# Kernel optimization log

Measured on AMD Instinct MI355X. Metric: run time of the kernel, lower is better.

Reference implementation:

```python
import jax, jax.numpy as jnp
import numpy as np

N, D, G = 16384, 2048, 4096  # points, vocab_size (feature dim), num_groups


def setup_inputs() -> dict:
    key = jax.random.key(0)
    kx, ke = jax.random.split(key)
    x = jax.random.normal(kx, (N, D), dtype=jnp.float32)
    # trunc_normal_ init for the codebook; plain normal is fine for a numeric reference
    emb = jax.random.truncated_normal(ke, -2.0, 2.0, (G, D), dtype=jnp.float32)
    return {"x": x, "emb": emb}


def reference(x, emb):
    x2 = jnp.sum(x * x, axis=-1, keepdims=True)          # [N, 1]
    e2 = jnp.sum(emb * emb, axis=-1)                     # [G]
    sq = x2 + e2[None, :] - 2.0 * (x @ emb.T)            # [N, G]
    dist = jnp.sqrt(jnp.maximum(sq, 0.0))
    return -dist
```

## Files before the change

### kernel.cpp

```cpp
#include <hip/hip_runtime.h>
#include <hip/hip_bf16.h>

#define NPTS 16384
#define DIM  2048
#define NGRP 4096
#define BK   32
#define NT   (DIM / BK)

typedef __bf16 bf16x8 __attribute__((ext_vector_type(8)));
typedef unsigned short u16x8 __attribute__((ext_vector_type(8)));
typedef float f32x4 __attribute__((ext_vector_type(4)));
typedef long long i64f8;

__device__ __forceinline__ unsigned short f2bf(float f) {
  union { float f; unsigned u; } v; v.f = f;
  unsigned u = v.u;
  return (unsigned short)((u + 0x7FFFu + ((u >> 16) & 1u)) >> 16);
}
__device__ __forceinline__ float bflo(unsigned u) { return __uint_as_float(u << 16); }
__device__ __forceinline__ float bfhi(unsigned u) { return __uint_as_float(u & 0xffff0000u); }

__device__ __forceinline__ unsigned cvtpk4(float a, float b, float c, float d) {
  int w = __builtin_amdgcn_cvt_pk_fp8_f32(a, b, 0, false);
  w = __builtin_amdgcn_cvt_pk_fp8_f32(c, d, w, true);
  return (unsigned)w;
}

__device__ __forceinline__ void gload16(const void* g, void* lds) {
  __builtin_amdgcn_global_load_lds(
      (const __attribute__((address_space(1))) unsigned*)g,
      (__attribute__((address_space(3))) unsigned*)lds, 16, 0, 0);
}

__device__ __forceinline__ bool sniff_bf16(const void* X) {
  const int lane = threadIdx.x & 63;
  unsigned hb = (((const unsigned short*)X)[lane] >> 8) & 0x7Fu;
  unsigned long long m = __ballot(hb >= 0x3Bu && hb <= 0x41u);
  return __popcll(m) >= 48;
}

__global__ __launch_bounds__(256) void prep_all_kernel(
    const void* __restrict__ Xin, const void* __restrict__ Ein,
    unsigned char* __restrict__ Xf8, unsigned char* __restrict__ Ef8,
    float* __restrict__ x2, float* __restrict__ e2) {
  const int lane  = threadIdx.x & 63;
  const int wavei = threadIdx.x >> 6;
  const bool isbf = sniff_bf16(Xin);

  const int grow = blockIdx.x * 4 + wavei;
  const void* in; unsigned char* q; float* nrm; int row;
  if (grow < NPTS) { in = Xin; q = Xf8; nrm = x2; row = grow; }
  else             { in = Ein; q = Ef8; nrm = e2; row = grow - NPTS; }

  unsigned char* qq = q + (size_t)row * DIM;
  float s = 0.f;
#pragma unroll
  for (int it = 0; it < 4; ++it) {
    float v0, v1, v2, v3, v4, v5, v6, v7;
    if (isbf) {
      const unsigned short* p = (const unsigned short*)in + (size_t)row * DIM;
      uint4 r = *(const uint4*)(p + it * 512 + lane * 8);
      v0 = bflo(r.x); v1 = bfhi(r.x); v2 = bflo(r.y); v3 = bfhi(r.y);
      v4 = bflo(r.z); v5 = bfhi(r.z); v6 = bflo(r.w); v7 = bfhi(r.w);
    } else {
      const float* p = (const float*)in + (size_t)row * DIM;
      float4 a = *(const float4*)(p + it * 512 + lane * 8);
      float4 b = *(const float4*)(p + it * 512 + lane * 8 + 4);
      v0 = a.x; v1 = a.y; v2 = a.z; v3 = a.w;
      v4 = b.x; v5 = b.y; v6 = b.z; v7 = b.w;
    }
    s += v0 * v0 + v1 * v1 + v2 * v2 + v3 * v3;
    s += v4 * v4 + v5 * v5 + v6 * v6 + v7 * v7;
    uint2 w;
    w.x = cvtpk4(v0, v1, v2, v3);
    w.y = cvtpk4(v4, v5, v6, v7);
    *(uint2*)(qq + it * 512 + lane * 8) = w;
  }
#pragma unroll
  for (int off = 32; off > 0; off >>= 1) s += __shfl_down(s, off, 64);
  if (lane == 0) nrm[row] = s;
}

__global__ __launch_bounds__(512, 2) void gemm_f8_kernel(
    const void* __restrict__ Xin,
    const unsigned char* __restrict__ X8, const unsigned char* __restrict__ E8,
    const float* __restrict__ x2, const float* __restrict__ e2,
    void* __restrict__ outv) {
  __shared__ __align__(16) unsigned char sbuf[4][16384];

  const int tid  = threadIdx.x;
  const int lane = tid & 63;
  const int wave = tid >> 6;
  const int wm   = wave >> 2;
  const int wn   = wave & 3;
  const int quad = lane >> 4;
  const int l16  = lane & 15;

  const bool isbf = sniff_bf16(Xin);

  const int rowBase = blockIdx.y * 256;
  const int colBase = blockIdx.x * 256;

  const size_t gA = (size_t)(rowBase + (tid >> 1)) * DIM + (tid & 1) * 16;
  const size_t gB = (size_t)(colBase + (tid >> 1)) * DIM + (tid & 1) * 16;

  const int aoff = (wm * 128 + l16) * 32 + quad * 8;
  const int boff = 8192 + (wn * 64 + l16) * 32 + quad * 8;

  f32x4 zero = {0.f, 0.f, 0.f, 0.f};
  f32x4 acc[8][4];
#pragma unroll
  for (int mt = 0; mt < 8; ++mt)
#pragma unroll
    for (int nt = 0; nt < 4; ++nt) acc[mt][nt] = zero;

  i64f8 a0[8], b0[4], a1[8], b1[4];

#define STAGE(t_) do {                                                          \
    gload16(X8 + gA + (size_t)(t_) * BK, &sbuf[(t_) & 3][wave * 1024]);         \
    gload16(E8 + gB + (size_t)(t_) * BK, &sbuf[(t_) & 3][8192 + wave * 1024]);  \
  } while (0)

#define DSR(t_, A_, B_) do { const unsigned char* sb_ = sbuf[(t_) & 3];         \
    _Pragma("unroll") for (int mt = 0; mt < 8; ++mt)                            \
      A_[mt] = *(const i64f8*)(const void*)(sb_ + aoff + mt * 512);             \
    _Pragma("unroll") for (int nt = 0; nt < 4; ++nt)                            \
      B_[nt] = *(const i64f8*)(const void*)(sb_ + boff + nt * 512);             \
  } while (0)

#define MFMA32(A_, B_) do {                                                     \
    __builtin_amdgcn_s_setprio(1);                                              \
    _Pragma("unroll") for (int mt = 0; mt < 8; ++mt)                            \
      _Pragma("unroll") for (int nt = 0; nt < 4; ++nt)                          \
        acc[mt][nt] = __builtin_amdgcn_mfma_f32_16x16x32_fp8_fp8(               \
            A_[mt], B_[nt], acc[mt][nt], 0, 0, 0);                              \
    __builtin_amdgcn_s_setprio(0);                                              \
    asm volatile("" ::: "memory");                                              \
  } while (0)

#define BODY(t_, DOSTAGE_, VMS_, A_, B_, DONEXT_, AN_, BN_, LKS_) do {          \
    asm volatile("s_waitcnt vmcnt(" VMS_ ")" ::: "memory");                     \
    __builtin_amdgcn_s_barrier();                                               \
    __builtin_amdgcn_sched_barrier(0);                                          \
    if (DOSTAGE_) STAGE((t_) + 3);                                              \
    if (DONEXT_) DSR((t_) + 1, AN_, BN_);                                       \
    __builtin_amdgcn_sched_barrier(0);                                          \
    asm volatile("s_waitcnt lgkmcnt(" LKS_ ")" ::: "memory");                   \
    __builtin_amdgcn_sched_barrier(0);                                          \
    MFMA32(A_, B_);                                                             \
  } while (0)

  STAGE(0); STAGE(1); STAGE(2);
  asm volatile("s_waitcnt vmcnt(4)" ::: "memory");
  __builtin_amdgcn_s_barrier();
  __builtin_amdgcn_sched_barrier(0);
  DSR(0, a0, b0);
  __builtin_amdgcn_sched_barrier(0);

#pragma unroll 1
  for (int p = 0; p < 29; ++p) {
    const int t = 2 * p;
    BODY(t,     true, "2", a0, b0, true, a1, b1, "12");
    BODY(t + 1, true, "2", a1, b1, true, a0, b0, "12");
  }
  BODY(58, true,  "2", a0, b0, true, a1, b1, "12");
  BODY(59, true,  "2", a1, b1, true, a0, b0, "12");
  BODY(60, true,  "2", a0, b0, true, a1, b1, "12");
  BODY(61, false, "2", a1, b1, true, a0, b0, "12");
  BODY(62, false, "0", a0, b0, true, a1, b1, "12");
  BODY(63, false, "0", a1, b1, false, a0, b0, "0");
#undef BODY
#undef MFMA32
#undef DSR
#undef STAGE

  float ec[4];
#pragma unroll
  for (int nt = 0; nt < 4; ++nt) ec[nt] = e2[colBase + wn * 64 + nt * 16 + l16];

  if (isbf) {
    unsigned short* out = (unsigned short*)outv;
#pragma unroll
    for (int mt = 0; mt < 8; ++mt)
#pragma unroll
      for (int r2 = 0; r2 < 4; ++r2) {
        const int row = rowBase + wm * 128 + mt * 16 + quad * 4 + r2;
        const float xr = x2[row];
#pragma unroll
        for (int nt = 0; nt < 4; ++nt) {
          const int col = colBase + wn * 64 + nt * 16 + l16;
          float sq = xr + ec[nt] - 2.0f * acc[mt][nt][r2];
          sq = sq > 0.f ? sq : 0.f;
          out[(size_t)row * NGRP + col] = f2bf(-__builtin_sqrtf(sq));
        }
      }
  } else {
    float* out = (float*)outv;
#pragma unroll
    for (int mt = 0; mt < 8; ++mt)
#pragma unroll
      for (int r2 = 0; r2 < 4; ++r2) {
        const int row = rowBase + wm * 128 + mt * 16 + quad * 4 + r2;
        const float xr = x2[row];
#pragma unroll
        for (int nt = 0; nt < 4; ++nt) {
          const int col = colBase + wn * 64 + nt * 16 + l16;
          float sq = xr + ec[nt] - 2.0f * acc[mt][nt][r2];
          sq = sq > 0.f ? sq : 0.f;
          out[(size_t)row * NGRP + col] = -__builtin_sqrtf(sq);
        }
      }
  }
}


__global__ void sniff_kernel(const unsigned short* __restrict__ X, int* __restrict__ flag) {
  if (threadIdx.x == 0 && blockIdx.x == 0) {
    int c = 0;
    for (int i = 0; i < 64; ++i) {
      unsigned b = (X[i] >> 8) & 0x7F;
      c += (b >= 0x3B && b <= 0x41) ? 1 : 0;
    }
    *flag = (c >= 48) ? 1 : 0;
  }
}

__global__ __launch_bounds__(256) void rownorm_kernel(const void* __restrict__ in,
                                                      float* __restrict__ out,
                                                      const int* __restrict__ flag) {
  const int wave = threadIdx.x >> 6;
  const int lane = threadIdx.x & 63;
  const int row  = blockIdx.x * 4 + wave;
  float s = 0.f;
  if (*flag) {
    const unsigned short* p = (const unsigned short*)in + (size_t)row * DIM;
#pragma unroll
    for (int it = 0; it < 4; ++it) {
      uint4 v = *(const uint4*)(p + it * 512 + lane * 8);
      float f;
      f = bflo(v.x); s += f * f;  f = bfhi(v.x); s += f * f;
      f = bflo(v.y); s += f * f;  f = bfhi(v.y); s += f * f;
      f = bflo(v.z); s += f * f;  f = bfhi(v.z); s += f * f;
      f = bflo(v.w); s += f * f;  f = bfhi(v.w); s += f * f;
    }
  } else {
    const float* p = (const float*)in + (size_t)row * DIM;
#pragma unroll
    for (int it = 0; it < 4; ++it) {
      float4 a = *(const float4*)(p + it * 512 + lane * 8);
      float4 b = *(const float4*)(p + it * 512 + lane * 8 + 4);
      s += a.x * a.x + a.y * a.y + a.z * a.z + a.w * a.w;
      s += b.x * b.x + b.y * b.y + b.z * b.z + b.w * b.w;
    }
  }
#pragma unroll
  for (int off = 32; off > 0; off >>= 1) s += __shfl_down(s, off, 64);
  if (lane == 0) out[row] = s;
}

__device__ __forceinline__ u16x8 cvt8(const float* p) {
  float4 a = *(const float4*)p;
  float4 b = *(const float4*)(p + 4);
  u16x8 r;
  r[0] = f2bf(a.x); r[1] = f2bf(a.y); r[2] = f2bf(a.z); r[3] = f2bf(a.w);
  r[4] = f2bf(b.x); r[5] = f2bf(b.y); r[6] = f2bf(b.z); r[7] = f2bf(b.w);
  return r;
}

__global__ __launch_bounds__(256) void gemm_dist_kernel(
    const void* __restrict__ Xv, const void* __restrict__ Ev,
    const float* __restrict__ x2, const float* __restrict__ e2,
    void* __restrict__ outv, const int* __restrict__ flag) {
  __shared__ __align__(16) unsigned short sA[128 * 32];
  __shared__ __align__(16) unsigned short sB[128 * 32];

  const bool isbf = (*flag != 0);
  const int tid  = threadIdx.x;
  const int lane = tid & 63;
  const int wave = tid >> 6;
  const int wm   = wave >> 1;
  const int wn   = wave & 1;
  const int quad = lane >> 4;
  const int l16  = lane & 15;

  const int rowBase = blockIdx.y * 128;
  const int colBase = blockIdx.x * 128;

  const int flat0 = tid * 8;
  const int flat1 = (tid + 256) * 8;
  const int r0 = flat0 >> 5, c0 = flat0 & 31;
  const int r1 = flat1 >> 5, c1 = flat1 & 31;

  const size_t iA0 = (size_t)(rowBase + r0) * DIM + c0;
  const size_t iA1 = (size_t)(rowBase + r1) * DIM + c1;
  const size_t iB0 = (size_t)(colBase + r0) * DIM + c0;
  const size_t iB1 = (size_t)(colBase + r1) * DIM + c1;

  f32x4 zero = {0.f, 0.f, 0.f, 0.f};
  f32x4 acc[4][4];
#pragma unroll
  for (int mt = 0; mt < 4; ++mt)
#pragma unroll
    for (int nt = 0; nt < 4; ++nt) acc[mt][nt] = zero;

  for (int k0 = 0; k0 < DIM; k0 += 32) {
    if (isbf) {
      const unsigned short* X = (const unsigned short*)Xv;
      const unsigned short* E = (const unsigned short*)Ev;
      *(uint4*)(sA + flat0) = *(const uint4*)(X + iA0 + k0);
      *(uint4*)(sA + flat1) = *(const uint4*)(X + iA1 + k0);
      *(uint4*)(sB + flat0) = *(const uint4*)(E + iB0 + k0);
      *(uint4*)(sB + flat1) = *(const uint4*)(E + iB1 + k0);
    } else {
      const float* X = (const float*)Xv;
      const float* E = (const float*)Ev;
      *(u16x8*)(sA + flat0) = cvt8(X + iA0 + k0);
      *(u16x8*)(sA + flat1) = cvt8(X + iA1 + k0);
      *(u16x8*)(sB + flat0) = cvt8(E + iB0 + k0);
      *(u16x8*)(sB + flat1) = cvt8(E + iB1 + k0);
    }
    __syncthreads();

    bf16x8 a[4], b[4];
#pragma unroll
    for (int mt = 0; mt < 4; ++mt)
      a[mt] = *(const bf16x8*)(const void*)(sA + (wm * 64 + mt * 16 + l16) * 32 + quad * 8);
#pragma unroll
    for (int nt = 0; nt < 4; ++nt)
      b[nt] = *(const bf16x8*)(const void*)(sB + (wn * 64 + nt * 16 + l16) * 32 + quad * 8);
#pragma unroll
    for (int mt = 0; mt < 4; ++mt)
#pragma unroll
      for (int nt = 0; nt < 4; ++nt)
        acc[mt][nt] = __builtin_amdgcn_mfma_f32_16x16x32_bf16(a[mt], b[nt], acc[mt][nt], 0, 0, 0);
    __syncthreads();
  }

  float ec[4];
#pragma unroll
  for (int nt = 0; nt < 4; ++nt) ec[nt] = e2[colBase + wn * 64 + nt * 16 + l16];

  if (isbf) {
    unsigned short* out = (unsigned short*)outv;
#pragma unroll
    for (int mt = 0; mt < 4; ++mt)
#pragma unroll
      for (int r = 0; r < 4; ++r) {
        const int row = rowBase + wm * 64 + mt * 16 + quad * 4 + r;
        const float xr = x2[row];
#pragma unroll
        for (int nt = 0; nt < 4; ++nt) {
          const int col = colBase + wn * 64 + nt * 16 + l16;
          float sq = xr + ec[nt] - 2.0f * acc[mt][nt][r];
          sq = sq > 0.f ? sq : 0.f;
          out[(size_t)row * NGRP + col] = f2bf(-__builtin_sqrtf(sq));
        }
      }
  } else {
    float* out = (float*)outv;
#pragma unroll
    for (int mt = 0; mt < 4; ++mt)
#pragma unroll
      for (int r = 0; r < 4; ++r) {
        const int row = rowBase + wm * 64 + mt * 16 + quad * 4 + r;
        const float xr = x2[row];
#pragma unroll
        for (int nt = 0; nt < 4; ++nt) {
          const int col = colBase + wn * 64 + nt * 16 + l16;
          float sq = xr + ec[nt] - 2.0f * acc[mt][nt][r];
          sq = sq > 0.f ? sq : 0.f;
          out[(size_t)row * NGRP + col] = -__builtin_sqrtf(sq);
        }
      }
  }
}

extern "C" void kernel_launch(void* const* d_in, const int* in_sizes, int n_in,
                              void* d_out, int out_size, void* d_ws, size_t ws_size,
                              hipStream_t stream) {
  const size_t xf8 = (size_t)NPTS * DIM;
  const size_t ef8 = (size_t)NGRP * DIM;
  const size_t need = xf8 + ef8 + (NPTS + NGRP) * sizeof(float) + 64;

  if (ws_size >= need) {
    unsigned char* Xf8 = (unsigned char*)d_ws;
    unsigned char* Ef8 = Xf8 + xf8;
    float* x2 = (float*)(Ef8 + ef8);
    float* e2 = x2 + NPTS;

    prep_all_kernel<<<(NPTS + NGRP) / 4, 256, 0, stream>>>(d_in[0], d_in[1],
                                                           Xf8, Ef8, x2, e2);
    dim3 grid(NGRP / 256, NPTS / 256);
    gemm_f8_kernel<<<grid, 512, 0, stream>>>(d_in[0], Xf8, Ef8, x2, e2, d_out);
  } else {
    float* x2 = (float*)d_ws;
    float* e2 = x2 + NPTS;
    int* flag = (int*)(e2 + NGRP);

    sniff_kernel<<<1, 64, 0, stream>>>((const unsigned short*)d_in[0], flag);
    rownorm_kernel<<<NPTS / 4, 256, 0, stream>>>(d_in[0], x2, flag);
    rownorm_kernel<<<NGRP / 4, 256, 0, stream>>>(d_in[1], e2, flag);
    dim3 grid(NGRP / 128, NPTS / 128);
    gemm_dist_kernel<<<grid, 256, 0, stream>>>(d_in[0], d_in[1], x2, e2, d_out, flag);
  }
}
```

Before: 614.9 us.

## Switch FP8 GEMM to MX-scaled 16x16x128 MFMA with swizzled K=128 tiles

Replaces the 16x16x32 fp8 MFMA loop with the gfx950 scaled f8f6f4 16x16x128 instruction, using unit E8M0 scales. K tiles grow to 128, and LDS staging moves to two 64KB buffers with an XOR-swizzled row layout so fragments can be read with wide loads. The pipeline is simplified to load fragments, run MFMAs, then issue the stage-after-next load. The intent is to double matrix throughput per instruction and cut the loop and barrier count. The larger LDS footprint likely limits the CU to one block, and load/compute overlap within a tile is reduced.

```diff
diff --git a/kernel.cpp b/kernel.cpp
--- a/kernel.cpp
+++ b/kernel.cpp
@@ -4,13 +4,14 @@
 #define NPTS 16384
 #define DIM  2048
 #define NGRP 4096
-#define BK   32
-#define NT   (DIM / BK)
+#define BKF  128
+#define NTF  (DIM / BKF)
 
 typedef __bf16 bf16x8 __attribute__((ext_vector_type(8)));
 typedef unsigned short u16x8 __attribute__((ext_vector_type(8)));
 typedef float f32x4 __attribute__((ext_vector_type(4)));
-typedef long long i64f8;
+typedef int i32x4 __attribute__((ext_vector_type(4)));
+typedef int i32x8 __attribute__((ext_vector_type(8)));
 
 __device__ __forceinline__ unsigned short f2bf(float f) {
   union { float f; unsigned u; } v; v.f = f;
@@ -81,12 +82,12 @@
   if (lane == 0) nrm[row] = s;
 }
 
-__global__ __launch_bounds__(512, 2) void gemm_f8_kernel(
+__global__ __launch_bounds__(512, 2) void gemm_mx_kernel(
     const void* __restrict__ Xin,
     const unsigned char* __restrict__ X8, const unsigned char* __restrict__ E8,
     const float* __restrict__ x2, const float* __restrict__ e2,
     void* __restrict__ outv) {
-  __shared__ __align__(16) unsigned char sbuf[4][16384];
+  __shared__ __align__(16) unsigned char sbuf[2][65536];
 
   const int tid  = threadIdx.x;
   const int lane = tid & 63;
@@ -101,77 +102,82 @@
   const int rowBase = blockIdx.y * 256;
   const int colBase = blockIdx.x * 256;
 
-  const size_t gA = (size_t)(rowBase + (tid >> 1)) * DIM + (tid & 1) * 16;
-  const size_t gB = (size_t)(colBase + (tid >> 1)) * DIM + (tid & 1) * 16;
-
-  const int aoff = (wm * 128 + l16) * 32 + quad * 8;
-  const int boff = 8192 + (wn * 64 + l16) * 32 + quad * 8;
-
-  f32x4 zero = {0.f, 0.f, 0.f, 0.f};
+  const int srow  = tid >> 3;
+  const int scol  = ((tid & 7) ^ (srow & 7)) * 16;
+  size_t gAo[4], gBo[4];
+#pragma unroll
+  for (int g = 0; g < 4; ++g) {
+    gAo[g] = (size_t)(rowBase + g * 64 + srow) * DIM + scol;
+    gBo[g] = (size_t)(colBase + g * 64 + srow) * DIM + scol;
+  }
+
+  const int cb0 = ((quad * 2) ^ (l16 & 7)) * 16;
+
   f32x4 acc[8][4];
 #pragma unroll
   for (int mt = 0; mt < 8; ++mt)
 #pragma unroll
-    for (int nt = 0; nt < 4; ++nt) acc[mt][nt] = zero;
-
-  i64f8 a0[8], b0[4], a1[8], b1[4];
-
-#define STAGE(t_) do {                                                          \
-    gload16(X8 + gA + (size_t)(t_) * BK, &sbuf[(t_) & 3][wave * 1024]);         \
-    gload16(E8 + gB + (size_t)(t_) * BK, &sbuf[(t_) & 3][8192 + wave * 1024]);  \
+    for (int nt = 0; nt < 4; ++nt) acc[mt][nt] = f32x4{0.f, 0.f, 0.f, 0.f};
+
+  i32x8 a8[4], b8[4];
+
+#define STAGE(t_) do { unsigned char* sb_ = sbuf[(t_) & 1];                     \
+    const size_t kk_ = (size_t)(t_) * BKF;                                      \
+    _Pragma("unroll") for (int g = 0; g < 4; ++g)                               \
+      gload16(X8 + gAo[g] + kk_, sb_ + g * 8192 + wave * 1024);                 \
+    _Pragma("unroll") for (int g = 0; g < 4; ++g)                               \
+      gload16(E8 + gBo[g] + kk_, sb_ + 32768 + g * 8192 + wave * 1024);         \
   } while (0)
 
-#define DSR(t_, A_, B_) do { const unsigned char* sb_ = sbuf[(t_) & 3];         \
-    _Pragma("unroll") for (int mt = 0; mt < 8; ++mt)                            \
-      A_[mt] = *(const i64f8*)(const void*)(sb_ + aoff + mt * 512);             \
-    _Pragma("unroll") for (int nt = 0; nt < 4; ++nt)                            \
-      B_[nt] = *(const i64f8*)(const void*)(sb_ + boff + nt * 512);             \
+#define LDFRAG(dst_, base_, rowi_) do {                                         \
+    const unsigned char* p_ = (base_) + (rowi_) * 128;                          \
+    i32x4 lo_ = *(const i32x4*)(const void*)(p_ + cb0);                         \
+    i32x4 hi_ = *(const i32x4*)(const void*)(p_ + (cb0 ^ 16));                  \
+    dst_[0] = lo_[0]; dst_[1] = lo_[1]; dst_[2] = lo_[2]; dst_[3] = lo_[3];     \
+    dst_[4] = hi_[0]; dst_[5] = hi_[1]; dst_[6] = hi_[2]; dst_[7] = hi_[3];     \
   } while (0)
 
-#define MFMA32(A_, B_) do {                                                     \
+#define MFMA16(MOFF_) do {                                                      \
     __builtin_amdgcn_s_setprio(1);                                              \
-    _Pragma("unroll") for (int mt = 0; mt < 8; ++mt)                            \
-      _Pragma("unroll") for (int nt = 0; nt < 4; ++nt)                          \
-        acc[mt][nt] = __builtin_amdgcn_mfma_f32_16x16x32_fp8_fp8(               \
-            A_[mt], B_[nt], acc[mt][nt], 0, 0, 0);                              \
+    _Pragma("unroll") for (int m = 0; m < 4; ++m)                               \
+      _Pragma("unroll") for (int n = 0; n < 4; ++n)                             \
+        acc[(MOFF_) + m][n] = __builtin_amdgcn_mfma_scale_f32_16x16x128_f8f6f4( \
+            a8[m], b8[n], acc[(MOFF_) + m][n], 0, 0,                            \
+            0, 0x7F7F7F7F, 0, 0x7F7F7F7F);           \
     __builtin_amdgcn_s_setprio(0);                                              \
-    asm volatile("" ::: "memory");                                              \
   } while (0)
 
-#define BODY(t_, DOSTAGE_, VMS_, A_, B_, DONEXT_, AN_, BN_, LKS_) do {          \
+#define BODY(t_, DOSTAGE_, VMS_) do {                                           \
     asm volatile("s_waitcnt vmcnt(" VMS_ ")" ::: "memory");                     \
     __builtin_amdgcn_s_barrier();                                               \
     __builtin_amdgcn_sched_barrier(0);                                          \
-    if (DOSTAGE_) STAGE((t_) + 3);                                              \
-    if (DONEXT_) DSR((t_) + 1, AN_, BN_);                                       \
+    const unsigned char* sa_ = sbuf[(t_) & 1];                                  \
+    const unsigned char* sb2_ = sa_ + 32768;                                    \
+    _Pragma("unroll") for (int m = 0; m < 4; ++m)                               \
+      LDFRAG(a8[m], sa_, (wm * 128 + m * 16 + l16));                            \
+    _Pragma("unroll") for (int n = 0; n < 4; ++n)                               \
+      LDFRAG(b8[n], sb2_, (wn * 64 + n * 16 + l16));                            \
+    MFMA16(0);                                                                  \
+    _Pragma("unroll") for (int m = 0; m < 4; ++m)                               \
+      LDFRAG(a8[m], sa_, (wm * 128 + (m + 4) * 16 + l16));                      \
+    MFMA16(4);                                                                  \
+    asm volatile("" ::: "memory");                                              \
+    __builtin_amdgcn_s_barrier();                                               \
     __builtin_amdgcn_sched_barrier(0);                                          \
-    asm volatile("s_waitcnt lgkmcnt(" LKS_ ")" ::: "memory");                   \
-    __builtin_amdgcn_sched_barrier(0);                                          \
-    MFMA32(A_, B_);                                                             \
+    if (DOSTAGE_) STAGE((t_) + 2);                                              \
   } while (0)
 
-  STAGE(0); STAGE(1); STAGE(2);
-  asm volatile("s_waitcnt vmcnt(4)" ::: "memory");
-  __builtin_amdgcn_s_barrier();
-  __builtin_amdgcn_sched_barrier(0);
-  DSR(0, a0, b0);
-  __builtin_amdgcn_sched_barrier(0);
+  STAGE(0); STAGE(1);
 
 #pragma unroll 1
-  for (int p = 0; p < 29; ++p) {
-    const int t = 2 * p;
-    BODY(t,     true, "2", a0, b0, true, a1, b1, "12");
-    BODY(t + 1, true, "2", a1, b1, true, a0, b0, "12");
-  }
-  BODY(58, true,  "2", a0, b0, true, a1, b1, "12");
-  BODY(59, true,  "2", a1, b1, true, a0, b0, "12");
-  BODY(60, true,  "2", a0, b0, true, a1, b1, "12");
-  BODY(61, false, "2", a1, b1, true, a0, b0, "12");
-  BODY(62, false, "0", a0, b0, true, a1, b1, "12");
-  BODY(63, false, "0", a1, b1, false, a0, b0, "0");
+  for (int t = 0; t < NTF - 2; ++t) {
+    BODY(t, true, "8");
+  }
+  BODY(NTF - 2, false, "8");
+  BODY(NTF - 1, false, "0");
 #undef BODY
-#undef MFMA32
-#undef DSR
+#undef MFMA16
+#undef LDFRAG
 #undef STAGE
 
   float ec[4];
@@ -391,7 +397,7 @@
     prep_all_kernel<<<(NPTS + NGRP) / 4, 256, 0, stream>>>(d_in[0], d_in[1],
                                                            Xf8, Ef8, x2, e2);
     dim3 grid(NGRP / 256, NPTS / 256);
-    gemm_f8_kernel<<<grid, 512, 0, stream>>>(d_in[0], Xf8, Ef8, x2, e2, d_out);
+    gemm_mx_kernel<<<grid, 512, 0, stream>>>(d_in[0], Xf8, Ef8, x2, e2, d_out);
   } else {
     float* x2 = (float*)d_ws;
     float* e2 = x2 + NPTS;
```

Measured after the change: 508.2 us, median of 3. 1.21x faster.
